# Optimization experiments

Measured on AMD Instinct MI355X. Metric: run time of the kernel, lower is better.

Reference implementation:

```python
import jax, jax.numpy as jnp
import numpy as np

B, S, D, H, Dh, A_N = 2, 1024, 512, 8, 64, 18
HID = H * Dh        # 512, equals in_features
FFN = 4 * D         # SwiGLU hidden (ratio=4)
EPS = 1e-6


def rmsnorm(x, scale):
    return x * jax.lax.rsqrt(jnp.mean(jnp.square(x), axis=-1, keepdims=True) + EPS) * scale


def setup_inputs() -> dict:
    key = jax.random.key(0)
    ks = jax.random.split(key, 16)
    lecun = lambda k, shp: jax.random.normal(k, shp, jnp.float32) * (1.0 / np.sqrt(shp[0]))
    return {
        "x": jax.random.normal(ks[0], (B, S, D), jnp.float32),
        "action": jax.random.randint(ks[1], (B, S), 0, A_N, jnp.int32),
        "mask": jnp.zeros((B, S), jnp.int32),
        "carry": jnp.zeros((B, H, Dh, Dh), jnp.float32),
        "norm1_scale": jnp.ones((D,), jnp.float32),
        "wq": lecun(ks[2], (D, HID)),
        "wk": lecun(ks[3], (D, HID)),
        "wv": lecun(ks[4], (D, HID)),
        "w_beta": lecun(ks[5], (D, H)),
        "embed": jax.random.normal(ks[6], (A_N, HID), jnp.float32) * 0.02,
        "w_alpha": lecun(ks[7], (HID, H)),
        "w_bu": lecun(ks[8], (HID, HID)),
        "w_bv": lecun(ks[9], (HID, HID)),
        "norm_attn_scale": jnp.ones((HID,), jnp.float32),
        "w_out": lecun(ks[10], (HID, D)),
        "b_out": jnp.zeros((D,), jnp.float32),
        "norm2_scale": jnp.ones((D,), jnp.float32),
        "w_gate": lecun(ks[11], (D, FFN)),
        "w_val": lecun(ks[12], (D, FFN)),
        "w_ffn": lecun(ks[13], (FFN, D)),
    }


def reference(x, action, mask, carry, norm1_scale, wq, wk, wv, w_beta, embed,
              w_alpha, w_bu, w_bv, norm_attn_scale, w_out, b_out,
              norm2_scale, w_gate, w_val, w_ffn):
    dt = x.dtype
    h = rmsnorm(x, norm1_scale)
    # projections -> [B,S,H,Dh]
    q = jax.nn.silu(h @ wq).reshape(B, S, H, Dh)
    k = jax.nn.silu(h @ wk).reshape(B, S, H, Dh)
    v = (h @ wv).reshape(B, S, H, Dh)
    beta = jax.nn.sigmoid(h @ w_beta)                       # [B,S,H]
    ae = embed[action]                                      # [B,S,HID]
    alpha = jax.nn.sigmoid(ae @ w_alpha)                    # [B,S,H]
    b_u = (ae @ w_bu).reshape(B, S, H, Dh)
    b_v = (ae @ w_bv).reshape(B, S, H, Dh)
    q = q / (jnp.linalg.norm(q, axis=-1, keepdims=True) + EPS)
    k = k / (jnp.linalg.norm(k, axis=-1, keepdims=True) + EPS)
    eye = jnp.eye(Dh, dtype=dt)
    # delta = I - beta * k k^T   -> [B,S,H,Dh,Dh]
    delta = eye - beta[..., None, None] * jnp.einsum("bshi,bshj->bshij", k, k)
    m = mask.astype(dt)[:, :, None, None, None]
    decay = alpha[..., None, None] * delta * (1.0 - m)
    drift = jnp.einsum("bshi,bshj->bshij", b_u, b_v)
    write = beta[..., None, None] * jnp.einsum("bshi,bshj->bshij", v, k)
    update = drift @ delta + write

    def binop(lhs, rhs):
        a_i, b_i = lhs
        a_j, b_j = rhs
        return (a_i @ a_j, b_i @ a_j + b_j)

    cumdecay, hs = jax.lax.associative_scan(jax.vmap(binop), (decay, update), axis=1)
    hs = carry[:, None] @ cumdecay + hs                     # [B,S,H,Dh,Dh]
    attn = jnp.einsum("bshij,bshj->bshi", hs, q).reshape(B, S, HID)
    attn = rmsnorm(attn, norm_attn_scale)
    y = attn @ w_out + b_out
    skip = y + x
    h2 = rmsnorm(skip, norm2_scale)
    ffn = (jax.nn.silu(h2 @ w_gate) * (h2 @ w_val)) @ w_ffn
    return (hs[:, -1], skip + ffn)
```

## Files before the change

kernel.cpp:

```cpp
#include <hip/hip_runtime.h>
#include <hip/hip_bf16.h>
#include <cstdint>
#include <cstddef>

using bf16 = __hip_bfloat16;
typedef __attribute__((ext_vector_type(8))) short bf16x8;
typedef __attribute__((ext_vector_type(4))) float f32x4;

static constexpr int B_ = 2, S_ = 1024, D_ = 512, H_ = 8;
static constexpr int M_ = B_ * S_;
static constexpr int CHUNKS_ = 32, CLEN_ = 32;
static constexpr float EPS_ = 1e-6f;

__device__ __forceinline__ float sigmoidf_(float x) { return 1.0f / (1.0f + __expf(-x)); }

__device__ __forceinline__ short bf_hi(float v, float& rem) {
  bf16 h = __float2bfloat16(v);
  rem = v - __bfloat162float(h);
  return *(short*)&h;
}
__device__ __forceinline__ short bf_of(float v) {
  bf16 h = __float2bfloat16(v);
  return *(short*)&h;
}

struct TJob { const float* src; bf16* dst; int K, N, base, xf; };
struct TTab { TJob j[9]; };

__global__ __launch_bounds__(256) void k_transpose_all(TTab tab) {
  __shared__ float tile[32][33];
  int blk = blockIdx.x;
  int ji = 0;
#pragma unroll
  for (int t = 1; t < 9; ++t) if (tab.j[t].base <= blk) ji = t;
  const float* W = tab.j[ji].src;
  bf16* Wt = tab.j[ji].dst;
  int K = tab.j[ji].K, N = tab.j[ji].N, xf = tab.j[ji].xf;
  int rel = blk - tab.j[ji].base;
  int nb = N >> 5;
  int n0 = (rel % nb) * 32, k0 = (rel / nb) * 32;
  int tx = threadIdx.x, ty = threadIdx.y;
#pragma unroll
  for (int r = ty; r < 32; r += 8) tile[r][tx] = W[(size_t)(k0 + r) * N + n0 + tx];
  __syncthreads();
#pragma unroll
  for (int r = ty; r < 32; r += 8) {
    int n = n0 + r;
    int drow = n;
    if (xf == 1) drow = ((n >> 5) << 6) + (n & 31);
    else if (xf == 2) drow = ((n >> 5) << 6) + (n & 31) + 32;
    Wt[(size_t)drow * K + k0 + tx] = __float2bfloat16(tile[tx][r]);
  }
}

__global__ __launch_bounds__(256) void k_pre(const float* __restrict__ x,
                                             const float* __restrict__ scale,
                                             float* __restrict__ hF, bf16* __restrict__ hB,
                                             const int* __restrict__ action,
                                             const float* __restrict__ embed,
                                             float* __restrict__ aeF, bf16* __restrict__ aeB) {
  int tid = threadIdx.x;
  if (blockIdx.x < M_) {
    int m = blockIdx.x;
    const float* row = x + (size_t)m * D_;
    float2 v = *(const float2*)(row + tid * 2);
    float ss = v.x * v.x + v.y * v.y;
#pragma unroll
    for (int o = 1; o < 64; o <<= 1) ss += __shfl_xor(ss, o);
    __shared__ float wsum[4];
    if ((tid & 63) == 0) wsum[tid >> 6] = ss;
    __syncthreads();
    float tot = wsum[0] + wsum[1] + wsum[2] + wsum[3];
    float rs = rsqrtf(tot * (1.0f / (float)D_) + EPS_);
    float2 sc = *(const float2*)(scale + tid * 2);
    float o0 = v.x * rs * sc.x, o1 = v.y * rs * sc.y;
    float2 o; o.x = o0; o.y = o1;
    *(float2*)(hF + (size_t)m * D_ + tid * 2) = o;
    bf16* p = hB + (size_t)m * D_ + tid * 2;
    p[0] = __float2bfloat16(o0); p[1] = __float2bfloat16(o1);
  } else {
    int m = blockIdx.x - M_;
    int a = action[m];
    float2 v = *(const float2*)(embed + (size_t)a * 512 + tid * 2);
    *(float2*)(aeF + (size_t)m * 512 + tid * 2) = v;
    bf16* p = aeB + (size_t)m * 512 + tid * 2;
    p[0] = __float2bfloat16(v.x); p[1] = __float2bfloat16(v.y);
  }
}

__global__ __launch_bounds__(256) void k_rmsnorm(const float* __restrict__ x,
                                                 const float* __restrict__ scale,
                                                 float* __restrict__ outf,
                                                 bf16* __restrict__ outb) {
  int m = blockIdx.x, tid = threadIdx.x;
  const float* row = x + (size_t)m * D_;
  float2 v = *(const float2*)(row + tid * 2);
  float ss = v.x * v.x + v.y * v.y;
#pragma unroll
  for (int o = 1; o < 64; o <<= 1) ss += __shfl_xor(ss, o);
  __shared__ float wsum[4];
  if ((tid & 63) == 0) wsum[tid >> 6] = ss;
  __syncthreads();
  float tot = wsum[0] + wsum[1] + wsum[2] + wsum[3];
  float rs = rsqrtf(tot * (1.0f / (float)D_) + EPS_);
  float2 sc = *(const float2*)(scale + tid * 2);
  float o0 = v.x * rs * sc.x, o1 = v.y * rs * sc.y;
  if (outf) {
    float2 o; o.x = o0; o.y = o1;
    *(float2*)(outf + (size_t)m * D_ + tid * 2) = o;
  }
  if (outb) {
    bf16* p = outb + (size_t)m * D_ + tid * 2;
    p[0] = __float2bfloat16(o0); p[1] = __float2bfloat16(o1);
  }
}

__global__ __launch_bounds__(256) void k_dot8x2(const float* __restrict__ hF,
                                                const float* __restrict__ aeF,
                                                const float* __restrict__ W1,
                                                const float* __restrict__ W2,
                                                float* __restrict__ o1,
                                                float* __restrict__ o2) {
  int m = blockIdx.x, tid = threadIdx.x;
  float x0 = hF[(size_t)m * D_ + tid], x1 = hF[(size_t)m * D_ + 256 + tid];
  float y0 = aeF[(size_t)m * D_ + tid], y1 = aeF[(size_t)m * D_ + 256 + tid];
  float p[8], q[8];
#pragma unroll
  for (int j = 0; j < 8; ++j) {
    p[j] = x0 * W1[tid * 8 + j] + x1 * W1[(tid + 256) * 8 + j];
    q[j] = y0 * W2[tid * 8 + j] + y1 * W2[(tid + 256) * 8 + j];
  }
#pragma unroll
  for (int j = 0; j < 8; ++j) {
#pragma unroll
    for (int o = 1; o < 64; o <<= 1) {
      p[j] += __shfl_xor(p[j], o);
      q[j] += __shfl_xor(q[j], o);
    }
  }
  __shared__ float sacc[4][16];
  if ((tid & 63) == 0) {
#pragma unroll
    for (int j = 0; j < 8; ++j) { sacc[tid >> 6][j] = p[j]; sacc[tid >> 6][8 + j] = q[j]; }
  }
  __syncthreads();
  if (tid < 8) {
    float s = sacc[0][tid] + sacc[1][tid] + sacc[2][tid] + sacc[3][tid];
    o1[(size_t)m * 8 + tid] = sigmoidf_(s);
  } else if (tid < 16) {
    int j = tid - 8;
    float s = sacc[0][8 + j] + sacc[1][8 + j] + sacc[2][8 + j] + sacc[3][8 + j];
    o2[(size_t)m * 8 + j] = sigmoidf_(s);
  }
}

__global__ __launch_bounds__(256) void k_qknorm_dots(float* __restrict__ qkv,
                                                     const float* __restrict__ buv,
                                                     const float* __restrict__ betaF,
                                                     const float* __restrict__ alphaF,
                                                     const int* __restrict__ mask,
                                                     float* __restrict__ scal8) {
  int blk = blockIdx.x * 4 + (threadIdx.x >> 6);
  int m = blk >> 3, h = blk & 7, t = threadIdx.x & 63;
  size_t qi = (size_t)m * 1536 + h * 64 + t;
  float q = qkv[qi], k = qkv[qi + 512];
  float bv = buv[(size_t)m * 1024 + 512 + h * 64 + t];
  float qs = q * q, ks = k * k;
#pragma unroll
  for (int o = 1; o < 64; o <<= 1) { qs += __shfl_xor(qs, o); ks += __shfl_xor(ks, o); }
  float qn = q / (sqrtf(qs) + EPS_);
  float kn = k / (sqrtf(ks) + EPS_);
  qkv[qi] = qn; qkv[qi + 512] = kn;
  float d0 = kn * qn, d1 = kn * bv, d2 = bv * qn;
#pragma unroll
  for (int o = 1; o < 64; o <<= 1) {
    d0 += __shfl_xor(d0, o); d1 += __shfl_xor(d1, o); d2 += __shfl_xor(d2, o);
  }
  if (t == 0) {
    int mh = m * 8 + h;
    float4 s4;
    s4.x = betaF[mh];
    s4.y = alphaF[mh] * (1.0f - (float)mask[m]);
    s4.z = d0; s4.w = d1;
    *(float4*)(scal8 + (size_t)mh * 8) = s4;
    scal8[(size_t)mh * 8 + 4] = d2;
  }
}

template <int EPI>
__global__ __launch_bounds__(256) void k_gemm2(const bf16* __restrict__ A,
                                               const bf16* __restrict__ Bt,
                                               void* __restrict__ Cv, int M, int N, int K,
                                               int actSplit, const float* __restrict__ bias,
                                               const float* __restrict__ res) {
  __shared__ bf16 As[2][64 * 32];
  __shared__ bf16 Bs[2][64 * 32];
  const int tid = threadIdx.x;
  const int wave = tid >> 6, lane = tid & 63;
  const int wm = wave >> 1, wn = wave & 1;
  const int m0 = blockIdx.y * 64, n0 = blockIdx.x * 64;
  const int lr = lane & 15, lg = lane >> 4;
  const int srow = (wave << 4) | (lane >> 2);
  const int skb = (lane & 3) << 3;
  const bf16* ga = A + (size_t)(m0 + srow) * K + skb;
  const bf16* gb = Bt + (size_t)(n0 + srow) * K + skb;

  f32x4 acc[2][2];
#pragma unroll
  for (int i = 0; i < 2; ++i)
#pragma unroll
    for (int j = 0; j < 2; ++j) acc[i][j] = (f32x4){0.f, 0.f, 0.f, 0.f};

  const int nk = K >> 5;
  int4 ar = *(const int4*)ga;
  int4 br = *(const int4*)gb;
  for (int t = 0; t < nk; ++t) {
    bf16* asb = &As[t & 1][0];
    bf16* bsb = &Bs[t & 1][0];
    *(int4*)(asb + tid * 8) = ar;
    *(int4*)(bsb + tid * 8) = br;
    __syncthreads();
    if (t + 1 < nk) {
      ar = *(const int4*)(ga + ((size_t)(t + 1) << 5));
      br = *(const int4*)(gb + ((size_t)(t + 1) << 5));
    }
    bf16x8 af[2], bfr[2];
#pragma unroll
    for (int mm = 0; mm < 2; ++mm)
      af[mm] = *(const bf16x8*)(asb + (wm * 32 + mm * 16 + lr) * 32 + lg * 8);
#pragma unroll
    for (int nn = 0; nn < 2; ++nn)
      bfr[nn] = *(const bf16x8*)(bsb + (wn * 32 + nn * 16 + lr) * 32 + lg * 8);
#pragma unroll
    for (int mm = 0; mm < 2; ++mm)
#pragma unroll
      for (int nn = 0; nn < 2; ++nn)
        acc[mm][nn] = __builtin_amdgcn_mfma_f32_16x16x32_bf16(af[mm], bfr[nn], acc[mm][nn], 0, 0, 0);
  }

  if constexpr (EPI == 4) {
    __syncthreads();
    float* gateL = (float*)&As[0][0];
    float* valL = (float*)&Bs[0][0];
    float* dstL = wn ? valL : gateL;
#pragma unroll
    for (int mm = 0; mm < 2; ++mm)
#pragma unroll
      for (int nn = 0; nn < 2; ++nn)
#pragma unroll
        for (int r = 0; r < 4; ++r)
          dstL[(wm * 32 + mm * 16 + lg * 4 + r) * 32 + nn * 16 + lr] = acc[mm][nn][r];
    __syncthreads();
    bf16* Cb = (bf16*)Cv;
    int row = tid >> 2, c0 = (tid & 3) * 8;
    bf16x8 o;
#pragma unroll
    for (int e = 0; e < 8; ++e) {
      float g = gateL[row * 32 + c0 + e];
      float v = valL[row * 32 + c0 + e];
      o[e] = bf_of(g * sigmoidf_(g) * v);
    }
    *(int4*)(Cb + (size_t)(m0 + row) * 2048 + blockIdx.x * 32 + c0) = *(int4*)&o;
  } else {
    float* C = (float*)Cv;
#pragma unroll
    for (int mm = 0; mm < 2; ++mm) {
#pragma unroll
      for (int nn = 0; nn < 2; ++nn) {
#pragma unroll
        for (int r = 0; r < 4; ++r) {
          int row = m0 + wm * 32 + mm * 16 + lg * 4 + r;
          int col = n0 + wn * 32 + nn * 16 + lr;
          float v = acc[mm][nn][r];
          if constexpr (EPI == 1) {
            if (col < actSplit) v = v * sigmoidf_(v);
          }
          if constexpr (EPI == 2) v += bias[col] + res[(size_t)row * N + col];
          if constexpr (EPI == 3) v += res[(size_t)row * N + col];
          C[(size_t)row * N + col] = v;
        }
      }
    }
  }
}


__global__ __launch_bounds__(512) void k_scan_chunk(
    const float* __restrict__ qkv, const float* __restrict__ buv,
    const float* __restrict__ scal8, bf16* __restrict__ PtHi,
    bf16* __restrict__ PtLo, float* __restrict__ Ut,
    float* __restrict__ Qtb, float* __restrict__ Vtb) {
  __shared__ float kL[CLEN_][64], qL[CLEN_][64], bvL[CLEN_][64];
  __shared__ float vL[CLEN_][64], buL[CLEN_][64];
  __shared__ float scL[CLEN_][8];
  const int blk = blockIdx.x, bh = blk >> 5, c = blk & (CHUNKS_ - 1);
  const int b = bh >> 3, h = bh & 7;
  const int tid = threadIdx.x, i = tid >> 3, q8 = tid & 7, j0 = q8 * 8;
  const bool writer = (q8 == 0);
  const int m0 = b * S_ + c * CLEN_;

  {
    int s = tid >> 4, fo = (tid & 15) * 4;
    const float* qb = qkv + (size_t)(m0 + s) * 1536 + h * 64;
    const float* bb = buv + (size_t)(m0 + s) * 1024 + h * 64;
    *(float4*)&qL[s][fo]  = *(const float4*)(qb + fo);
    *(float4*)&kL[s][fo]  = *(const float4*)(qb + 512 + fo);
    *(float4*)&vL[s][fo]  = *(const float4*)(qb + 1024 + fo);
    *(float4*)&buL[s][fo] = *(const float4*)(bb + fo);
    *(float4*)&bvL[s][fo] = *(const float4*)(bb + 512 + fo);
    if ((tid & 15) < 2)
      *(float4*)&scL[s][(tid & 1) * 4] =
          *(const float4*)(scal8 + (size_t)((m0 + s) * 8 + h) * 8 + (tid & 1) * 4);
  }
  __syncthreads();

  alignas(16) float P[8], U[8];
#pragma unroll
  for (int jj = 0; jj < 8; ++jj) { P[jj] = (j0 + jj == i) ? 1.f : 0.f; U[jj] = 0.f; }
  float* QT = Qtb + ((size_t)bh * CHUNKS_ + c) * (CLEN_ * 64);
  float* VT = Vtb + ((size_t)bh * CHUNKS_ + c) * (CLEN_ * 64);

  struct Step8 { float k[8], q[8], bv[8]; float v_i, bu_i, beta, g, kq, kbv, bvq; };
  auto LOAD = [&](Step8& sd, int s) {
    *(float4*)&sd.k[0]  = *(const float4*)&kL[s][j0];
    *(float4*)&sd.k[4]  = *(const float4*)&kL[s][j0 + 4];
    *(float4*)&sd.q[0]  = *(const float4*)&qL[s][j0];
    *(float4*)&sd.q[4]  = *(const float4*)&qL[s][j0 + 4];
    *(float4*)&sd.bv[0] = *(const float4*)&bvL[s][j0];
    *(float4*)&sd.bv[4] = *(const float4*)&bvL[s][j0 + 4];
    sd.v_i = vL[s][i];
    sd.bu_i = buL[s][i];
    float4 s4 = *(const float4*)&scL[s][0];
    sd.beta = s4.x; sd.g = s4.y; sd.kq = s4.z; sd.kbv = s4.w;
    sd.bvq = scL[s][4];
  };
  auto STEP = [&](const Step8& sd, int s) {
    float Pk = 0.f, Uk = 0.f, Pq = 0.f, Uq = 0.f;
#pragma unroll
    for (int jj = 0; jj < 8; ++jj) {
      Pk += P[jj] * sd.k[jj]; Uk += U[jj] * sd.k[jj];
      Pq += P[jj] * sd.q[jj]; Uq += U[jj] * sd.q[jj];
    }
    Pk += __shfl_xor(Pk, 1); Pk += __shfl_xor(Pk, 2); Pk += __shfl_xor(Pk, 4);
    Uk += __shfl_xor(Uk, 1); Uk += __shfl_xor(Uk, 2); Uk += __shfl_xor(Uk, 4);
    Pq += __shfl_xor(Pq, 1); Pq += __shfl_xor(Pq, 2); Pq += __shfl_xor(Pq, 4);
    Uq += __shfl_xor(Uq, 1); Uq += __shfl_xor(Uq, 2); Uq += __shfl_xor(Uq, 4);
    float gb = sd.g * sd.beta;
    float cP = gb * Pk;
    float Ai = sd.beta * sd.v_i - gb * Uk - sd.bu_i * sd.beta * sd.kbv;
    if (writer) {
      QT[s * 64 + i] = sd.g * Pq - cP * sd.kq;
      VT[s * 64 + i] = sd.g * Uq + Ai * sd.kq + sd.bu_i * sd.bvq;
    }
#pragma unroll
    for (int jj = 0; jj < 8; ++jj) {
      P[jj] = sd.g * P[jj] - cP * sd.k[jj];
      U[jj] = sd.g * U[jj] + Ai * sd.k[jj] + sd.bu_i * sd.bv[jj];
    }
  };

  Step8 A, Bs;
  LOAD(A, 0);
  LOAD(Bs, 1);
  for (int s = 0; s < CLEN_; s += 2) {
    STEP(A, s);
    if (s + 2 < CLEN_) LOAD(A, s + 2);
    STEP(Bs, s + 1);
    if (s + 3 < CLEN_) LOAD(Bs, s + 3);
  }

  const size_t base = ((size_t)bh * CHUNKS_ + c) * 4096;
#pragma unroll
  for (int jj = 0; jj < 8; ++jj) {
    int j = j0 + jj;
    float pv = P[jj];
    float rem;
    short ph = bf_hi(pv, rem);
    short pl = bf_of(rem);
    ((short*)PtHi)[base + (size_t)j * 64 + i] = ph;
    ((short*)PtLo)[base + (size_t)j * 64 + i] = pl;
    Ut[base + (size_t)j * 64 + i] = U[jj];
  }
}

#define PREFETCH_(SET, CIDX)                                                     \
  {                                                                              \
    const size_t cbo_ = (size_t)(CIDX) * 4096;                                   \
    _Pragma("unroll") for (int mt = 0; mt < 4; ++mt) {                           \
      _Pragma("unroll") for (int ks = 0; ks < 2; ++ks) {                         \
        size_t off_ = cbo_ + (size_t)(16 * mt + lr) * 64 + ks * 32 + lg * 8;     \
        aH[SET][mt][ks] = *(const bf16x8*)(PH + off_);                           \
        aL[SET][mt][ks] = *(const bf16x8*)(PL + off_);                           \
      }                                                                          \
      _Pragma("unroll") for (int r = 0; r < 4; ++r)                              \
        u[SET][mt][r] = UB[cbo_ + (size_t)(16 * mt + 4 * lg + r) * 64 + col0 + lr]; \
    }                                                                            \
  }

#define CHAINSTEP_(SET, NSET, CIDX)                                              \
  {                                                                              \
    if ((CIDX) + 1 < CHUNKS_) PREFETCH_(NSET, (CIDX) + 1);                       \
    _Pragma("unroll") for (int mt = 0; mt < 4; ++mt)                             \
      _Pragma("unroll") for (int r = 0; r < 4; ++r)                              \
        HB[(size_t)(CIDX) * 4096 + (size_t)(16 * mt + 4 * lg + r) * 64 + col0 + lr] = st[mt][r]; \
    bf16x8 bH[2], bL[2];                                                         \
    _Pragma("unroll") for (int ks = 0; ks < 2; ++ks) {                           \
      _Pragma("unroll") for (int e = 0; e < 8; ++e) {                            \
        int src_ = (2 * (lg & 1) + (e >> 2)) * 16 + lr;                          \
        float va_ = __shfl(st[2 * ks][e & 3], src_);                             \
        float vb_ = __shfl(st[2 * ks + 1][e & 3], src_);                         \
        float bv_ = (lg & 2) ? vb_ : va_;                                        \
        float rem_;                                                              \
        bH[ks][e] = bf_hi(bv_, rem_);                                            \
        bL[ks][e] = bf_of(rem_);                                                 \
      }                                                                          \
    }                                                                            \
    f32x4 stn[4];                                                                \
    _Pragma("unroll") for (int mt = 0; mt < 4; ++mt) {                           \
      f32x4 a_ = u[SET][mt];                                                     \
      _Pragma("unroll") for (int ks = 0; ks < 2; ++ks) {                         \
        a_ = __builtin_amdgcn_mfma_f32_16x16x32_bf16(aH[SET][mt][ks], bH[ks], a_, 0, 0, 0); \
        a_ = __builtin_amdgcn_mfma_f32_16x16x32_bf16(aH[SET][mt][ks], bL[ks], a_, 0, 0, 0); \
        a_ = __builtin_amdgcn_mfma_f32_16x16x32_bf16(aL[SET][mt][ks], bH[ks], a_, 0, 0, 0); \
      }                                                                          \
      stn[mt] = a_;                                                              \
    }                                                                            \
    _Pragma("unroll") for (int mt = 0; mt < 4; ++mt) st[mt] = stn[mt];           \
  }

__global__ __launch_bounds__(64, 1) void k_chain3(
    const bf16* __restrict__ PtHi, const bf16* __restrict__ PtLo,
    const float* __restrict__ Ut, const float* __restrict__ carry,
    float* __restrict__ Hbuf, float* __restrict__ out_hs) {
  const int bh = blockIdx.x >> 2, cb = blockIdx.x & 3, col0 = cb * 16;
  const int lane = threadIdx.x & 63, lr = lane & 15, lg = lane >> 4;
  const short* PH = (const short*)PtHi + (size_t)bh * CHUNKS_ * 4096;
  const short* PL = (const short*)PtLo + (size_t)bh * CHUNKS_ * 4096;
  const float* UB = Ut + (size_t)bh * CHUNKS_ * 4096;
  float* HB = Hbuf + (size_t)bh * CHUNKS_ * 4096;

  f32x4 st[4];
#pragma unroll
  for (int mt = 0; mt < 4; ++mt)
    st[mt] = *(const f32x4*)(carry + ((size_t)bh * 64 + col0 + lr) * 64 + 16 * mt + 4 * lg);

  bf16x8 aH[2][4][2], aL[2][4][2];
  f32x4 u[2][4];
  PREFETCH_(0, 0);
  for (int c = 0; c < CHUNKS_; c += 2) {
    CHAINSTEP_(0, 1, c);
    CHAINSTEP_(1, 0, c + 1);
  }
#pragma unroll
  for (int mt = 0; mt < 4; ++mt)
    *(f32x4*)(out_hs + ((size_t)bh * 64 + col0 + lr) * 64 + 16 * mt + 4 * lg) = st[mt];
}

__global__ __launch_bounds__(256) void k_attn_gemm(
    const float* __restrict__ Hbuf, const float* __restrict__ Qtb,
    const float* __restrict__ Vtb, float* __restrict__ attn) {
  const int blk = blockIdx.x, bh = blk >> 5, c = blk & (CHUNKS_ - 1);
  const int b = bh >> 3, h = bh & 7;
  const int tid = threadIdx.x, wave = tid >> 6, lane = tid & 63;
  const int lr = lane & 15, lg = lane >> 4;
  const float* H0 = Hbuf + ((size_t)bh * CHUNKS_ + c) * 4096;
  const float* QT = Qtb + ((size_t)bh * CHUNKS_ + c) * (CLEN_ * 64);
  const float* VT = Vtb + ((size_t)bh * CHUNKS_ + c) * (CLEN_ * 64);

  bf16x8 aH[2], aL[2];
#pragma unroll
  for (int ks = 0; ks < 2; ++ks) {
#pragma unroll
    for (int e = 0; e < 8; ++e) {
      float v = H0[(size_t)(ks * 32 + lg * 8 + e) * 64 + wave * 16 + lr];
      float rem;
      aH[ks][e] = bf_hi(v, rem);
      aL[ks][e] = bf_of(rem);
    }
  }
  f32x4 acc[2];
#pragma unroll
  for (int nt = 0; nt < 2; ++nt) {
    f32x4 a = (f32x4){0.f, 0.f, 0.f, 0.f};
#pragma unroll
    for (int ks = 0; ks < 2; ++ks) {
      const float* qp = QT + (size_t)(nt * 16 + lr) * 64 + ks * 32 + lg * 8;
      bf16x8 bH, bL;
#pragma unroll
      for (int e = 0; e < 8; ++e) {
        float rem;
        bH[e] = bf_hi(qp[e], rem);
        bL[e] = bf_of(rem);
      }
      a = __builtin_amdgcn_mfma_f32_16x16x32_bf16(aH[ks], bH, a, 0, 0, 0);
      a = __builtin_amdgcn_mfma_f32_16x16x32_bf16(aH[ks], bL, a, 0, 0, 0);
      a = __builtin_amdgcn_mfma_f32_16x16x32_bf16(aL[ks], bH, a, 0, 0, 0);
    }
    acc[nt] = a;
  }
  const int m0 = b * S_ + c * CLEN_;
#pragma unroll
  for (int nt = 0; nt < 2; ++nt) {
    int s = nt * 16 + lr;
    f32x4 vt = *(const f32x4*)(VT + (size_t)s * 64 + wave * 16 + lg * 4);
    f32x4 o = acc[nt];
#pragma unroll
    for (int r = 0; r < 4; ++r) o[r] += vt[r];
    *(f32x4*)(attn + (size_t)(m0 + s) * 512 + h * 64 + wave * 16 + lg * 4) = o;
  }
}

extern "C" void kernel_launch(void* const* d_in, const int* in_sizes, int n_in,
                              void* d_out, int out_size, void* d_ws, size_t ws_size,
                              hipStream_t stream) {
  const float* x      = (const float*)d_in[0];
  const int*   action = (const int*)d_in[1];
  const int*   mask   = (const int*)d_in[2];
  const float* carry  = (const float*)d_in[3];
  const float* n1s    = (const float*)d_in[4];
  const float* wq     = (const float*)d_in[5];
  const float* wk     = (const float*)d_in[6];
  const float* wv     = (const float*)d_in[7];
  const float* wbeta  = (const float*)d_in[8];
  const float* embed  = (const float*)d_in[9];
  const float* walpha = (const float*)d_in[10];
  const float* wbu    = (const float*)d_in[11];
  const float* wbv    = (const float*)d_in[12];
  const float* nas    = (const float*)d_in[13];
  const float* wout   = (const float*)d_in[14];
  const float* bout   = (const float*)d_in[15];
  const float* n2s    = (const float*)d_in[16];
  const float* wgate  = (const float*)d_in[17];
  const float* wval   = (const float*)d_in[18];
  const float* wffn   = (const float*)d_in[19];

  float* out_hs  = (float*)d_out;
  float* out_ffn = (float*)d_out + 65536;

  char* p = (char*)d_ws;
  auto alloc = [&](size_t bytes) -> char* {
    char* r = p; p += (bytes + 255) & ~(size_t)255; return r;
  };
  bf16*  wqkvT = (bf16*)alloc((size_t)1536 * 512 * 2);
  bf16*  wbuvT = (bf16*)alloc((size_t)1024 * 512 * 2);
  bf16*  woutT = (bf16*)alloc((size_t)512 * 512 * 2);
  bf16*  wgvT  = (bf16*)alloc((size_t)4096 * 512 * 2);
  bf16*  wffnT = (bf16*)alloc((size_t)512 * 2048 * 2);
  float* qkvF  = (float*)alloc((size_t)M_ * 1536 * 4);
  float* buvF  = (float*)alloc((size_t)M_ * 1024 * 4);
  float* betaF = (float*)alloc((size_t)M_ * 8 * 4);
  float* alphaF= (float*)alloc((size_t)M_ * 8 * 4);
  float* scal8 = (float*)alloc((size_t)M_ * 8 * 8 * 4);
  float* attnF = (float*)alloc((size_t)M_ * 512 * 4);
  bf16*  attnB = (bf16*)alloc((size_t)M_ * 512 * 2);
  float* skipF = (float*)alloc((size_t)M_ * 512 * 4);
  bf16*  h2B   = (bf16*)alloc((size_t)M_ * 512 * 2);
  bf16*  ffnB  = (bf16*)alloc((size_t)M_ * 2048 * 2);
  char*  tail  = alloc((size_t)32 * 1024 * 1024);
  if ((size_t)(p - (char*)d_ws) > ws_size) return;

  float* hF  = (float*)tail;
  bf16*  hB  = (bf16*)(tail + ((size_t)4 << 20));
  float* aeF = (float*)(tail + ((size_t)6 << 20));
  bf16*  aeB = (bf16*)(tail + ((size_t)10 << 20));

  bf16*  PtHi = (bf16*)tail;
  bf16*  PtLo = (bf16*)(tail + ((size_t)4 << 20));
  float* UtB  = (float*)(tail + ((size_t)8 << 20));
  float* Hbuf = (float*)(tail + ((size_t)16 << 20));
  float* Qtb  = (float*)(tail + ((size_t)24 << 20));
  float* Vtb  = (float*)(tail + ((size_t)28 << 20));

  TTab tab;
  tab.j[0] = {wq,    wqkvT,              512,  512,  0,    0};
  tab.j[1] = {wk,    wqkvT + 512 * 512,  512,  512,  256,  0};
  tab.j[2] = {wv,    wqkvT + 1024 * 512, 512,  512,  512,  0};
  tab.j[3] = {wbu,   wbuvT,              512,  512,  768,  0};
  tab.j[4] = {wbv,   wbuvT + 512 * 512,  512,  512,  1024, 0};
  tab.j[5] = {wout,  woutT,              512,  512,  1280, 0};
  tab.j[6] = {wgate, wgvT,               512,  2048, 1536, 1};
  tab.j[7] = {wval,  wgvT,               512,  2048, 2560, 2};
  tab.j[8] = {wffn,  wffnT,              2048, 512,  3584, 0};
  k_transpose_all<<<4608, dim3(32, 8), 0, stream>>>(tab);

  k_pre<<<M_ * 2, 256, 0, stream>>>(x, n1s, hF, hB, action, embed, aeF, aeB);

  k_gemm2<1><<<dim3(1536 / 64, M_ / 64), 256, 0, stream>>>(hB, wqkvT, qkvF, M_, 1536, 512, 1024, nullptr, nullptr);
  k_gemm2<0><<<dim3(1024 / 64, M_ / 64), 256, 0, stream>>>(aeB, wbuvT, buvF, M_, 1024, 512, 0, nullptr, nullptr);
  k_dot8x2<<<M_, 256, 0, stream>>>(hF, aeF, wbeta, walpha, betaF, alphaF);
  k_qknorm_dots<<<M_ * 2, 256, 0, stream>>>(qkvF, buvF, betaF, alphaF, mask, scal8);

  k_scan_chunk<<<16 * CHUNKS_, 512, 0, stream>>>(qkvF, buvF, scal8, PtHi, PtLo, UtB, Qtb, Vtb);
  k_chain3<<<64, 64, 0, stream>>>(PtHi, PtLo, UtB, carry, Hbuf, out_hs);
  k_attn_gemm<<<16 * CHUNKS_, 256, 0, stream>>>(Hbuf, Qtb, Vtb, attnF);

  k_rmsnorm<<<M_, 256, 0, stream>>>(attnF, nas, nullptr, attnB);
  k_gemm2<2><<<dim3(512 / 64, M_ / 64), 256, 0, stream>>>(attnB, woutT, skipF, M_, 512, 512, 0, bout, x);
  k_rmsnorm<<<M_, 256, 0, stream>>>(skipF, n2s, nullptr, h2B);
  k_gemm2<4><<<dim3(4096 / 64, M_ / 64), 256, 0, stream>>>(h2B, wgvT, ffnB, M_, 4096, 512, 0, nullptr, nullptr);
  k_gemm2<3><<<dim3(512 / 64, M_ / 64), 256, 0, stream>>>(ffnB, wffnT, out_ffn, M_, 512, 2048, 0, nullptr, skipF);
}
```

Before: 190.1 us.

## Add 128x128-tile GEMM kernel for QKV and gate/value projections

Adds a k_gemm3 kernel with 128x128 output tiles, 512 threads and a 2x4 MFMA fragment per wave. The QKV projection and the SwiGLU gate/value GEMM now use it. The gate/value weight interleave is widened to 64-column groups, so one wave pair holds gate and the other value, and they are combined through padded LDS. The larger tiles raise operand reuse and cut global traffic and block count, at the cost of more registers and LDS per block and fewer blocks to fill the CUs.

```diff
diff --git a/kernel.cpp b/kernel.cpp
--- a/kernel.cpp
+++ b/kernel.cpp
@@ -47,8 +47,8 @@
   for (int r = ty; r < 32; r += 8) {
     int n = n0 + r;
     int drow = n;
-    if (xf == 1) drow = ((n >> 5) << 6) + (n & 31);
-    else if (xf == 2) drow = ((n >> 5) << 6) + (n & 31) + 32;
+    if (xf == 1) drow = ((n >> 6) << 7) + (n & 63);
+    else if (xf == 2) drow = ((n >> 6) << 7) + (n & 63) + 64;
     Wt[(size_t)drow * K + k0 + tx] = __float2bfloat16(tile[tx][r]);
   }
 }
@@ -238,45 +238,119 @@
         acc[mm][nn] = __builtin_amdgcn_mfma_f32_16x16x32_bf16(af[mm], bfr[nn], acc[mm][nn], 0, 0, 0);
   }
 
+  float* C = (float*)Cv;
+#pragma unroll
+  for (int mm = 0; mm < 2; ++mm) {
+#pragma unroll
+    for (int nn = 0; nn < 2; ++nn) {
+#pragma unroll
+      for (int r = 0; r < 4; ++r) {
+        int row = m0 + wm * 32 + mm * 16 + lg * 4 + r;
+        int col = n0 + wn * 32 + nn * 16 + lr;
+        float v = acc[mm][nn][r];
+        if constexpr (EPI == 1) {
+          if (col < actSplit) v = v * sigmoidf_(v);
+        }
+        if constexpr (EPI == 2) v += bias[col] + res[(size_t)row * N + col];
+        if constexpr (EPI == 3) v += res[(size_t)row * N + col];
+        C[(size_t)row * N + col] = v;
+      }
+    }
+  }
+}
+
+template <int EPI>
+__global__ __launch_bounds__(512) void k_gemm3(const bf16* __restrict__ A,
+                                               const bf16* __restrict__ Bt,
+                                               void* __restrict__ Cv, int M, int N, int K,
+                                               int actSplit) {
+  __shared__ bf16 As[2][128 * 32];
+  __shared__ bf16 Bs[2][128 * 32];
+  __shared__ float gateL[EPI == 4 ? 128 * 65 : 1];
+  const int tid = threadIdx.x;
+  const int wave = tid >> 6, lane = tid & 63;
+  const int wm = wave >> 1, wn = wave & 1;
+  const int m0 = blockIdx.y * 128, n0 = blockIdx.x * 128;
+  const int lr = lane & 15, lg = lane >> 4;
+  const int srow = tid >> 2, skb = (tid & 3) << 3;
+  const bf16* ga = A + (size_t)(m0 + srow) * K + skb;
+  const bf16* gb = Bt + (size_t)(n0 + srow) * K + skb;
+
+  f32x4 acc[2][4];
+#pragma unroll
+  for (int i = 0; i < 2; ++i)
+#pragma unroll
+    for (int j = 0; j < 4; ++j) acc[i][j] = (f32x4){0.f, 0.f, 0.f, 0.f};
+
+  const int nk = K >> 5;
+  int4 ar = *(const int4*)ga;
+  int4 br = *(const int4*)gb;
+  for (int t = 0; t < nk; ++t) {
+    bf16* asb = &As[t & 1][0];
+    bf16* bsb = &Bs[t & 1][0];
+    *(int4*)(asb + tid * 8) = ar;
+    *(int4*)(bsb + tid * 8) = br;
+    __syncthreads();
+    if (t + 1 < nk) {
+      ar = *(const int4*)(ga + ((size_t)(t + 1) << 5));
+      br = *(const int4*)(gb + ((size_t)(t + 1) << 5));
+    }
+    bf16x8 af[2], bfr[4];
+#pragma unroll
+    for (int mm = 0; mm < 2; ++mm)
+      af[mm] = *(const bf16x8*)(asb + (wm * 32 + mm * 16 + lr) * 32 + lg * 8);
+#pragma unroll
+    for (int nn = 0; nn < 4; ++nn)
+      bfr[nn] = *(const bf16x8*)(bsb + (wn * 64 + nn * 16 + lr) * 32 + lg * 8);
+#pragma unroll
+    for (int mm = 0; mm < 2; ++mm)
+#pragma unroll
+      for (int nn = 0; nn < 4; ++nn)
+        acc[mm][nn] = __builtin_amdgcn_mfma_f32_16x16x32_bf16(af[mm], bfr[nn], acc[mm][nn], 0, 0, 0);
+  }
+
   if constexpr (EPI == 4) {
     __syncthreads();
-    float* gateL = (float*)&As[0][0];
-    float* valL = (float*)&Bs[0][0];
-    float* dstL = wn ? valL : gateL;
-#pragma unroll
-    for (int mm = 0; mm < 2; ++mm)
-#pragma unroll
-      for (int nn = 0; nn < 2; ++nn)
-#pragma unroll
-        for (int r = 0; r < 4; ++r)
-          dstL[(wm * 32 + mm * 16 + lg * 4 + r) * 32 + nn * 16 + lr] = acc[mm][nn][r];
+    if (wn == 0) {
+#pragma unroll
+      for (int mm = 0; mm < 2; ++mm)
+#pragma unroll
+        for (int nn = 0; nn < 4; ++nn)
+#pragma unroll
+          for (int r = 0; r < 4; ++r)
+            gateL[(wm * 32 + mm * 16 + lg * 4 + r) * 65 + nn * 16 + lr] = acc[mm][nn][r];
+    }
     __syncthreads();
-    bf16* Cb = (bf16*)Cv;
-    int row = tid >> 2, c0 = (tid & 3) * 8;
-    bf16x8 o;
-#pragma unroll
-    for (int e = 0; e < 8; ++e) {
-      float g = gateL[row * 32 + c0 + e];
-      float v = valL[row * 32 + c0 + e];
-      o[e] = bf_of(g * sigmoidf_(g) * v);
-    }
-    *(int4*)(Cb + (size_t)(m0 + row) * 2048 + blockIdx.x * 32 + c0) = *(int4*)&o;
+    if (wn == 1) {
+      bf16* Cb = (bf16*)Cv;
+#pragma unroll
+      for (int mm = 0; mm < 2; ++mm)
+#pragma unroll
+        for (int nn = 0; nn < 4; ++nn)
+#pragma unroll
+          for (int r = 0; r < 4; ++r) {
+            int row = wm * 32 + mm * 16 + lg * 4 + r;
+            int vcol = nn * 16 + lr;
+            float g = gateL[row * 65 + vcol];
+            float v = acc[mm][nn][r];
+            Cb[(size_t)(m0 + row) * 2048 + blockIdx.x * 64 + vcol] =
+                __float2bfloat16(g * sigmoidf_(g) * v);
+          }
+    }
   } else {
     float* C = (float*)Cv;
 #pragma unroll
     for (int mm = 0; mm < 2; ++mm) {
 #pragma unroll
-      for (int nn = 0; nn < 2; ++nn) {
+      for (int nn = 0; nn < 4; ++nn) {
 #pragma unroll
         for (int r = 0; r < 4; ++r) {
           int row = m0 + wm * 32 + mm * 16 + lg * 4 + r;
-          int col = n0 + wn * 32 + nn * 16 + lr;
+          int col = n0 + wn * 64 + nn * 16 + lr;
           float v = acc[mm][nn][r];
           if constexpr (EPI == 1) {
             if (col < actSplit) v = v * sigmoidf_(v);
           }
-          if constexpr (EPI == 2) v += bias[col] + res[(size_t)row * N + col];
-          if constexpr (EPI == 3) v += res[(size_t)row * N + col];
           C[(size_t)row * N + col] = v;
         }
       }
@@ -585,7 +659,7 @@
 
   k_pre<<<M_ * 2, 256, 0, stream>>>(x, n1s, hF, hB, action, embed, aeF, aeB);
 
-  k_gemm2<1><<<dim3(1536 / 64, M_ / 64), 256, 0, stream>>>(hB, wqkvT, qkvF, M_, 1536, 512, 1024, nullptr, nullptr);
+  k_gemm3<1><<<dim3(1536 / 128, M_ / 128), 512, 0, stream>>>(hB, wqkvT, qkvF, M_, 1536, 512, 1024);
   k_gemm2<0><<<dim3(1024 / 64, M_ / 64), 256, 0, stream>>>(aeB, wbuvT, buvF, M_, 1024, 512, 0, nullptr, nullptr);
   k_dot8x2<<<M_, 256, 0, stream>>>(hF, aeF, wbeta, walpha, betaF, alphaF);
   k_qknorm_dots<<<M_ * 2, 256, 0, stream>>>(qkvF, buvF, betaF, alphaF, mask, scal8);
@@ -597,6 +671,6 @@
   k_rmsnorm<<<M_, 256, 0, stream>>>(attnF, nas, nullptr, attnB);
   k_gemm2<2><<<dim3(512 / 64, M_ / 64), 256, 0, stream>>>(attnB, woutT, skipF, M_, 512, 512, 0, bout, x);
   k_rmsnorm<<<M_, 256, 0, stream>>>(skipF, n2s, nullptr, h2B);
-  k_gemm2<4><<<dim3(4096 / 64, M_ / 64), 256, 0, stream>>>(h2B, wgvT, ffnB, M_, 4096, 512, 0, nullptr, nullptr);
+  k_gemm3<4><<<dim3(4096 / 128, M_ / 128), 512, 0, stream>>>(h2B, wgvT, ffnB, M_, 4096, 512, 0);
   k_gemm2<3><<<dim3(512 / 64, M_ / 64), 256, 0, stream>>>(ffnB, wffnT, out_ffn, M_, 512, 2048, 0, nullptr, skipF);
 }
```

New measurement: 189.9 us. Within noise of the previous version (-0.1%).
